# Performance work log

Measured on AMD Instinct MI355X. Metric: run time of the kernel, lower is better.

The kernel has to match this reference:

```python
import jax, jax.numpy as jnp
import numpy as np

H = 32; L = 4; HEADS = 8; VC = 16; BIG = 1e9

def _unit(v):
    return v * jax.lax.rsqrt(jnp.sum(v * v, -1, keepdims=True) + 1e-8)

def _dihedrals(bb):
    n = bb.shape[0]
    X = bb[:, :3].reshape(n * 3, 3)
    U = _unit(X[1:] - X[:-1])
    u2, u1, u0 = U[:-2], U[1:-1], U[2:]
    n2 = _unit(jnp.cross(u2, u1)); n1 = _unit(jnp.cross(u1, u0))
    cosD = jnp.clip(jnp.sum(n2 * n1, -1), -1 + 1e-6, 1 - 1e-6)
    D = jnp.sign(jnp.sum(u2 * n1, -1)) * jnp.arccos(cosD)
    D = jnp.pad(D, (1, 2)).reshape(n, 3)
    return jnp.concatenate([jnp.cos(D), jnp.sin(D)], -1)

def _orientations(x):
    f = jnp.pad(_unit(x[1:] - x[:-1]), ((0, 1), (0, 0)))
    b = jnp.pad(_unit(x[:-1] - x[1:]), ((1, 0), (0, 0)))
    return jnp.stack([f, b], -2)

def _virtual_cb(bb):
    n_, ca, c = bb[:, 0], bb[:, 1], bb[:, 2]
    b = ca - n_; cc = c - ca; a = jnp.cross(b, cc)
    return -0.58273431 * a + 0.56802827 * b - 0.54067466 * cc + ca

def _rbf(d, nbin=16, dmax=20.0):
    mu = jnp.linspace(0.0, dmax, nbin); sig = dmax / nbin
    return jnp.exp(-(((d[..., None] - mu) / sig) ** 2))

def _pos_emb(didx, nemb=16):
    freq = jnp.exp(jnp.arange(0, nemb, 2, dtype=jnp.float32) * (-np.log(10000.0) / nemb))
    ang = didx[..., None].astype(jnp.float32) * freq
    return jnp.concatenate([jnp.cos(ang), jnp.sin(ang)], -1)

def _edge_rot(vec):
    # per-edge rotation aligning edge direction to e_y (equiformer-style)
    nrm = _unit(vec)
    helper = jnp.where(jnp.abs(nrm[..., 2:3]) > 0.99, jnp.array([1.0, 0.0, 0.0]), jnp.array([0.0, 0.0, 1.0]))
    z = _unit(jnp.cross(nrm, helper))
    x = jnp.cross(nrm, z)
    return jnp.stack([x, nrm, z], axis=-2)

def _rot(R, x):
    return jnp.concatenate([x[..., :1, :], jnp.einsum('...ij,...jc->...ic', R, x[..., 1:, :])], -2)

def _rot_inv(R, x):
    return jnp.concatenate([x[..., :1, :], jnp.einsum('...ji,...jc->...ic', R, x[..., 1:, :])], -2)

def _norm_so3(x, g0, b0, g1):
    x0 = x[..., 0, :]; x1 = x[..., 1:, :]
    mu = jnp.mean(x0, -1, keepdims=True)
    var = jnp.var(x0, -1, keepdims=True)
    y0 = (x0 - mu) * jax.lax.rsqrt(var + 1e-6) * g0 + b0
    y1 = x1 * jax.lax.rsqrt(jnp.mean(x1 * x1, (-2, -1), keepdims=True) + 1e-6) * g1
    return jnp.concatenate([y0[..., None, :], y1], -2)

def _project(xin, nbr, R, ef, rw1, rw2, ow):
    src = _rot(R, xin[nbr])                         # [N,k,4,Cin] gather + rotate into edge frame
    rad = jax.nn.silu(ef @ rw1) @ rw2               # [N,k,Cin] radial weights
    msg = _rot_inv(R, src * rad[..., None, :])      # rotate back to global frame
    return jnp.mean(msg, axis=1) @ ow               # [N,4,Cout]

def _forward(bb, latent, ln_g0, ln_b0, ln_g1, bb_rad_w1, bb_rad_w2, bb_out_w,
             lat_rad_w1, lat_rad_w2, lat_out_w, tln_g0, tln_b0, tln_g1,
             attn_w1, attn_w2, v_w, o_w, ffn_w1, ffn_w2, ffn_wg, ffn_v1,
             eu_w1, eu_w2, out_rad_w1, out_rad_w2, out_w,
             seq_w1, seq_b1, seq_w2, seq_b2, seq_w3, seq_b3, x_mask, n_per, k):
    N = bb.shape[0]
    Xca = bb[:, 1]
    # backbone SO3 features [N,4,7]: l=0 dihedrals (padded to 7), l=1 seven vectors
    dih = jnp.pad(_dihedrals(bb), ((0, 0), (0, 1)))
    vecs = jnp.concatenate([bb - Xca[:, None], _orientations(Xca),
                            (_virtual_cb(bb) - Xca)[:, None]], -2)
    bb_feat = jnp.concatenate([dih[:, None, :], jnp.nan_to_num(jnp.swapaxes(vecs, -1, -2))], 1)
    # kNN graph within each chain; masked residues pushed far away
    batch = jnp.arange(N) // n_per
    mx = jnp.where(x_mask[:, None], BIG, Xca)
    sq = jnp.sum(mx * mx, -1)
    d2 = sq[:, None] + sq[None, :] - 2.0 * (mx @ mx.T)
    bad = (batch[:, None] != batch[None, :]) | jnp.eye(N, dtype=bool)
    d2 = jnp.where(bad, BIG, d2)
    _, nbr = jax.lax.top_k(-d2, k)                  # [N,k] source indices per target
    edge_vec = Xca[:, None] - Xca[nbr]
    R = _edge_rot(edge_vec)                         # [N,k,3,3]
    dist = jnp.sqrt(jnp.sum(edge_vec * edge_vec, -1) + 1e-12)
    ef = jnp.concatenate([_rbf(dist), _pos_emb(nbr - jnp.arange(N)[:, None])], -1)  # [N,k,32]
    lat = _norm_so3(latent, ln_g0, ln_b0, ln_g1)
    x = jnp.concatenate([_project(bb_feat, nbr, R, ef, bb_rad_w1, bb_rad_w2, bb_out_w),
                         _project(lat, nbr, R, ef, lat_rad_w1, lat_rad_w2, lat_out_w)], -1)  # [N,4,H]
    for l in range(L):
        xl = _norm_so3(x, tln_g0[l], tln_b0[l], tln_g1[l])
        src = xl[nbr]                               # [N,k,4,H]
        feat = jnp.concatenate([src[..., 0, :],
                                jnp.broadcast_to(xl[:, None, 0, :], src[..., 0, :].shape),
                                ef], -1)            # [N,k,3H]
        alpha = jax.nn.softmax(jax.nn.silu(feat @ attn_w1[l]) @ attn_w2[l], axis=1)  # [N,k,heads]
        v = _rot_inv(R, _rot(R, src) @ v_w[l])      # [N,k,4,heads*vc]
        v = v.reshape(N, k, 4, HEADS, VC)
        agg = jnp.einsum('nkh,nkchv->nchv', alpha, v).reshape(N, 4, HEADS * VC)
        x = x + agg @ o_w[l]
        h = jax.nn.silu(x[:, 0, :] @ ffn_w1[l])
        gate = jax.nn.sigmoid(h @ ffn_wg[l])
        x = x + jnp.concatenate([(h @ ffn_w2[l])[:, None, :],
                                 (x[:, 1:, :] @ ffn_v1[l]) * gate[:, None, :]], 1)
        e_in = jnp.concatenate([ef, x[nbr][..., 0, :],
                                jnp.broadcast_to(x[:, None, 0, :], (N, k, H))], -1)
        ef = ef + jax.nn.silu(e_in @ eu_w1[l]) @ eu_w2[l]
    atoms = _project(x, nbr, R, ef, out_rad_w1, out_rad_w2, out_w)  # [N,4,91]
    decoded_latent = jnp.swapaxes(atoms[:, 1:4, :], -1, -2)         # [N,91,3]
    hh = jax.nn.relu(x[:, 0, :] @ seq_w1 + seq_b1)
    hh = jax.nn.relu(hh @ seq_w2 + seq_b2)
    seq_logits = jax.nn.log_softmax(hh @ seq_w3 + seq_b3, -1)
    return decoded_latent, seq_logits

def setup_inputs() -> dict:
    key = jax.random.key(0)
    N = 8192; n_per = 2048; k = 30
    keys = iter(jax.random.split(key, 64))
    def W(shape):
        fan = shape[-2] if len(shape) > 1 else shape[-1]
        return (jax.random.normal(next(keys), shape) / np.sqrt(fan)).astype(jnp.float32)
    inp = {
        'bb': (jax.random.normal(next(keys), (N, 4, 3)) * 3.0).astype(jnp.float32),
        'latent': jax.random.normal(next(keys), (N, 4, H), dtype=jnp.float32),
        'ln_g0': jnp.ones((H,), jnp.float32), 'ln_b0': jnp.zeros((H,), jnp.float32), 'ln_g1': jnp.ones((H,), jnp.float32),
        'bb_rad_w1': W((H, 64)), 'bb_rad_w2': W((64, 7)), 'bb_out_w': W((7, 16)),
        'lat_rad_w1': W((H, 64)), 'lat_rad_w2': W((64, H)), 'lat_out_w': W((H, 16)),
        'tln_g0': jnp.ones((L, H), jnp.float32), 'tln_b0': jnp.zeros((L, H), jnp.float32), 'tln_g1': jnp.ones((L, H), jnp.float32),
        'attn_w1': W((L, 3 * H, H)), 'attn_w2': W((L, H, HEADS)),
        'v_w': W((L, H, HEADS * VC)), 'o_w': W((L, HEADS * VC, H)),
        'ffn_w1': W((L, H, 2 * H)), 'ffn_w2': W((L, 2 * H, H)), 'ffn_wg': W((L, 2 * H, H)), 'ffn_v1': W((L, H, H)),
        'eu_w1': W((L, 3 * H, 2 * H)), 'eu_w2': W((L, 2 * H, H)),
        'out_rad_w1': W((H, 64)), 'out_rad_w2': W((64, H)), 'out_w': W((H, 91)),
        'seq_w1': W((H, 64)), 'seq_b1': jnp.zeros((64,), jnp.float32),
        'seq_w2': W((64, H)), 'seq_b2': jnp.zeros((H,), jnp.float32),
        'seq_w3': W((H, 20)), 'seq_b3': jnp.zeros((20,), jnp.float32),
        'x_mask': jnp.zeros((N,), bool), 'n_per': n_per, 'k': k,
    }
    return inp

def reference(bb, latent, ln_g0, ln_b0, ln_g1, bb_rad_w1, bb_rad_w2, bb_out_w,
              lat_rad_w1, lat_rad_w2, lat_out_w, tln_g0, tln_b0, tln_g1,
              attn_w1, attn_w2, v_w, o_w, ffn_w1, ffn_w2, ffn_wg, ffn_v1,
              eu_w1, eu_w2, out_rad_w1, out_rad_w2, out_w,
              seq_w1, seq_b1, seq_w2, seq_b2, seq_w3, seq_b3, x_mask, n_per, k):
    return _forward(bb, latent, ln_g0, ln_b0, ln_g1, bb_rad_w1, bb_rad_w2, bb_out_w,
                    lat_rad_w1, lat_rad_w2, lat_out_w, tln_g0, tln_b0, tln_g1,
                    attn_w1, attn_w2, v_w, o_w, ffn_w1, ffn_w2, ffn_wg, ffn_v1,
                    eu_w1, eu_w2, out_rad_w1, out_rad_w2, out_w,
                    seq_w1, seq_b1, seq_w2, seq_b2, seq_w3, seq_b3, x_mask, n_per, k)
```

## Files before the change

### kernel.cpp

```cpp
#include <hip/hip_runtime.h>
#include <math.h>

#define NRES 8192
#define NPER 2048
#define KNB  30
#define NEDGE (NRES*KNB)

typedef float v2f __attribute__((ext_vector_type(2)));

__device__ __forceinline__ float siluf(float x){ return x / (1.0f + __expf(-x)); }
__device__ __forceinline__ v2f splat2(float a){ v2f r; r.x=a; r.y=a; return r; }

__global__ void k_bbfeat(const float* __restrict__ bb, float* __restrict__ bbf,
                         float4* __restrict__ ca){
  int n = blockIdx.x*256 + threadIdx.x;
  if(n >= NRES) return;
  const float* r = bb + n*12;
  float cax=r[3], cay=r[4], caz=r[5];
  ca[n] = make_float4(cax,cay,caz, cax*cax+cay*cay+caz*caz);
  float vx[7],vy[7],vz[7];
  for(int a=0;a<4;a++){ vx[a]=r[a*3]-cax; vy[a]=r[a*3+1]-cay; vz[a]=r[a*3+2]-caz; }
  if(n<NRES-1){
    float dx=bb[(n+1)*12+3]-cax, dy=bb[(n+1)*12+4]-cay, dz=bb[(n+1)*12+5]-caz;
    float s=rsqrtf(dx*dx+dy*dy+dz*dz+1e-8f);
    vx[4]=dx*s; vy[4]=dy*s; vz[4]=dz*s;
  } else { vx[4]=0.f; vy[4]=0.f; vz[4]=0.f; }
  if(n>0){
    float dx=bb[(n-1)*12+3]-cax, dy=bb[(n-1)*12+4]-cay, dz=bb[(n-1)*12+5]-caz;
    float s=rsqrtf(dx*dx+dy*dy+dz*dz+1e-8f);
    vx[5]=dx*s; vy[5]=dy*s; vz[5]=dz*s;
  } else { vx[5]=0.f; vy[5]=0.f; vz[5]=0.f; }
  {
    float bx=cax-r[0], by=cay-r[1], bz=caz-r[2];
    float cx=r[6]-cax, cy=r[7]-cay, cz=r[8]-caz;
    float axx=by*cz-bz*cy, ayy=bz*cx-bx*cz, azz=bx*cy-by*cx;
    vx[6]=-0.58273431f*axx+0.56802827f*bx-0.54067466f*cx;
    vy[6]=-0.58273431f*ayy+0.56802827f*by-0.54067466f*cy;
    vz[6]=-0.58273431f*azz+0.56802827f*bz-0.54067466f*cz;
  }
  float cD[3], sD[3];
  for(int t=0;t<3;t++){
    cD[t]=1.0f; sD[t]=0.0f;
    int f=3*n+t-1;
    if(f>=0 && f<3*NRES-3){
      float X[4][3];
      for(int q=0;q<4;q++){
        int m=f+q, rr=m/3, aa=m-rr*3;
        X[q][0]=bb[rr*12+aa*3]; X[q][1]=bb[rr*12+aa*3+1]; X[q][2]=bb[rr*12+aa*3+2];
      }
      float u2x=X[1][0]-X[0][0], u2y=X[1][1]-X[0][1], u2z=X[1][2]-X[0][2];
      float u1x=X[2][0]-X[1][0], u1y=X[2][1]-X[1][1], u1z=X[2][2]-X[1][2];
      float u0x=X[3][0]-X[2][0], u0y=X[3][1]-X[2][1], u0z=X[3][2]-X[2][2];
      float s2=rsqrtf(u2x*u2x+u2y*u2y+u2z*u2z+1e-8f); u2x*=s2; u2y*=s2; u2z*=s2;
      float s1=rsqrtf(u1x*u1x+u1y*u1y+u1z*u1z+1e-8f); u1x*=s1; u1y*=s1; u1z*=s1;
      float s0=rsqrtf(u0x*u0x+u0y*u0y+u0z*u0z+1e-8f); u0x*=s0; u0y*=s0; u0z*=s0;
      float n2x=u2y*u1z-u2z*u1y, n2y=u2z*u1x-u2x*u1z, n2z=u2x*u1y-u2y*u1x;
      float nn2=rsqrtf(n2x*n2x+n2y*n2y+n2z*n2z+1e-8f); n2x*=nn2; n2y*=nn2; n2z*=nn2;
      float n1x=u1y*u0z-u1z*u0y, n1y=u1z*u0x-u1x*u0z, n1z=u1x*u0y-u1y*u0x;
      float nn1=rsqrtf(n1x*n1x+n1y*n1y+n1z*n1z+1e-8f); n1x*=nn1; n1y*=nn1; n1z*=nn1;
      float dotn = n2x*n1x+n2y*n1y+n2z*n1z;
      float cosD = fminf(fmaxf(dotn, -1.0f+1e-6f), 1.0f-1e-6f);
      float sg = u2x*n1x+u2y*n1y+u2z*n1z;
      if(sg==0.0f){ cD[t]=1.0f; sD[t]=0.0f; }
      else {
        float sgn = (sg>0.0f)?1.0f:-1.0f;
        cD[t]=cosD;
        sD[t]=sgn*sqrtf(fmaxf(1.0f-cosD*cosD,0.0f));
      }
    }
  }
  float* o = bbf + n*28;
  o[0]=cD[0]; o[1]=cD[1]; o[2]=cD[2]; o[3]=sD[0]; o[4]=sD[1]; o[5]=sD[2]; o[6]=0.f;
  for(int c=0;c<7;c++){ o[7+c]=vx[c]; o[14+c]=vy[c]; o[21+c]=vz[c]; }
}

__device__ __forceinline__ unsigned long long knn_extract(const float* __restrict__ vals,
                                                          unsigned &mask, int lane){
  float bm=INFINITY; int ba=0;
  #pragma unroll
  for(int t=0;t<32;t++){
    if(!((mask>>t)&1u) && vals[t]<bm){ bm=vals[t]; ba=t; }
  }
  mask |= 1u<<ba;
  unsigned ub = __float_as_uint(bm);
  ub ^= (ub & 0x80000000u) ? 0xFFFFFFFFu : 0x80000000u;
  return ((unsigned long long)ub<<32) | (unsigned)(ba*64+lane);
}

__global__ __launch_bounds__(256) void k_knn(const float4* __restrict__ ca, int* __restrict__ nbr){
  __shared__ float sx[NPER], sy[NPER], sz[NPER], sq[NPER];
  int wave = threadIdx.x>>6;
  int lane = threadIdx.x&63;
  int i = blockIdx.x*4 + wave;
  int batch = i / NPER;
  int base = batch*NPER;
  for(int t=threadIdx.x; t<NPER; t+=256){
    float4 c = ca[base+t];
    sx[t]=c.x; sy[t]=c.y; sz[t]=c.z; sq[t]=c.w;
  }
  __syncthreads();
  int il = i - base;
  float xi=sx[il], yi=sy[il], zi=sz[il], si=sq[il];
  float vals[32];
  #pragma unroll
  for(int t=0;t<32;t++){
    int j = t*64 + lane;
    float d2 = si + sq[j] - 2.0f*(xi*sx[j]+yi*sy[j]+zi*sz[j]);
    if(j==il) d2 = 1e30f;
    vals[t]=d2;
  }
  unsigned mask = 0;
  unsigned long long s0 = knn_extract(vals, mask, lane);
  unsigned long long s1 = knn_extract(vals, mask, lane);
  unsigned long long s2 = knn_extract(vals, mask, lane);
  unsigned long long s3 = knn_extract(vals, mask, lane);
  const unsigned long long EMPTY = ~0ull;
  for(int it=0; it<KNB; it++){
    unsigned long long m = s0;
    #pragma unroll
    for(int off=32; off>0; off>>=1){
      unsigned long long o = __shfl_xor(m, off, 64);
      m = (o<m) ? o : m;
    }
    if(lane==0) nbr[i*KNB+it] = base + (int)(m & 0x7FFull);
    if((int)(m & 63ull) == lane){
      s0=s1; s1=s2; s2=s3; s3=EMPTY;
      if(s0==EMPTY) s0 = knn_extract(vals, mask, lane);
    }
  }
}

__global__ void k_tbl(float* __restrict__ tbl){
  int i = blockIdx.x*256 + threadIdx.x;
  int d = i>>3, m = i&7;
  float freq = __expf(-1.1512925465f*(float)m);
  float ang = (float)(d-2048)*freq;
  tbl[d*16+m]   = cosf(ang);
  tbl[d*16+8+m] = sinf(ang);
}

__global__ __launch_bounds__(128, 4)
void k_edgerad(const float4* __restrict__ ca, const int* __restrict__ nbr,
               const float* __restrict__ tbl,
               const float* __restrict__ bbw1, const float* __restrict__ bbw2,
               const float* __restrict__ latw1, const float* __restrict__ latw2,
               float* __restrict__ ef, float* __restrict__ radbb, float* __restrict__ radlat){
  int e = blockIdx.x*128 + threadIdx.x;
  int n = e/KNB;
  int j = nbr[e];
  float4 cn = ca[n], cj = ca[j];
  float dx=cn.x-cj.x, dy=cn.y-cj.y, dz=cn.z-cj.z;
  float dist = sqrtf(dx*dx+dy*dy+dz*dz + 1e-12f);
  float f[32];
  #pragma unroll
  for(int m=0;m<16;m++){
    float mu = (20.0f/15.0f)*(float)m;
    float t = (dist-mu)*(1.0f/1.25f);
    f[m] = __expf(-t*t);
  }
  {
    const float4* t4 = (const float4*)(tbl + (size_t)(j - n + 2048)*16);
    float4 c0=t4[0], c1=t4[1], s0=t4[2], s1=t4[3];
    f[16]=c0.x; f[17]=c0.y; f[18]=c0.z; f[19]=c0.w;
    f[20]=c1.x; f[21]=c1.y; f[22]=c1.z; f[23]=c1.w;
    f[24]=s0.x; f[25]=s0.y; f[26]=s0.z; f[27]=s0.w;
    f[28]=s1.x; f[29]=s1.y; f[30]=s1.z; f[31]=s1.w;
  }
  {
    float4* o4 = (float4*)(ef + (size_t)e*32);
    #pragma unroll
    for(int q=0;q<8;q++) o4[q] = make_float4(f[q*4],f[q*4+1],f[q*4+2],f[q*4+3]);
  }
  float ab[7];
  #pragma unroll
  for(int t=0;t<7;t++) ab[t]=0.f;
  #pragma unroll
  for(int half=0; half<2; half++){
    v2f h[16];
    #pragma unroll
    for(int o=0;o<16;o++) h[o]=splat2(0.f);
    #pragma unroll
    for(int c=0;c<32;c++){
      v2f fc = splat2(f[c]);
      const v2f* w = (const v2f*)(bbw1 + c*64 + half*32);
      #pragma unroll
      for(int o=0;o<16;o++) h[o] += fc*w[o];
    }
    #pragma unroll
    for(int o=0;o<16;o++){
      float v0 = siluf(h[o].x), v1 = siluf(h[o].y);
      const float* wa = bbw2 + (half*32+o*2)*7;
      const float* wb = bbw2 + (half*32+o*2+1)*7;
      #pragma unroll
      for(int t=0;t<7;t++) ab[t] += v0*wa[t];
      #pragma unroll
      for(int t=0;t<7;t++) ab[t] += v1*wb[t];
    }
  }
  {
    float4* rb4 = (float4*)(radbb + (size_t)e*8);
    rb4[0] = make_float4(ab[0],ab[1],ab[2],ab[3]);
    rb4[1] = make_float4(ab[4],ab[5],ab[6],0.f);
  }
  v2f al[16];
  #pragma unroll
  for(int t=0;t<16;t++) al[t]=splat2(0.f);
  #pragma unroll
  for(int half=0; half<2; half++){
    v2f h[16];
    #pragma unroll
    for(int o=0;o<16;o++) h[o]=splat2(0.f);
    #pragma unroll
    for(int c=0;c<32;c++){
      v2f fc = splat2(f[c]);
      const v2f* w = (const v2f*)(latw1 + c*64 + half*32);
      #pragma unroll
      for(int o=0;o<16;o++) h[o] += fc*w[o];
    }
    #pragma unroll
    for(int o=0;o<16;o++){
      float v0 = siluf(h[o].x), v1 = siluf(h[o].y);
      const v2f* wa = (const v2f*)(latw2 + (half*32+o*2)*32);
      const v2f* wb = (const v2f*)(latw2 + (half*32+o*2+1)*32);
      v2f va = splat2(v0), vb = splat2(v1);
      #pragma unroll
      for(int t=0;t<16;t++) al[t] += va*wa[t];
      #pragma unroll
      for(int t=0;t<16;t++) al[t] += vb*wb[t];
    }
  }
  v2f* rl2 = (v2f*)(radlat + (size_t)e*32);
  #pragma unroll
  for(int q=0;q<16;q++) rl2[q] = al[q];
}

__global__ void k_norm(const float* __restrict__ in, float* __restrict__ out,
                       const float* __restrict__ g0, const float* __restrict__ b0,
                       const float* __restrict__ g1){
  int tid = blockIdx.x*256 + threadIdx.x;
  int n = tid >> 5, lane = tid & 31;
  if(n >= NRES) return;
  const float* xn = in + n*128;
  float x0 = xn[lane];
  float s = x0, s2 = x0*x0;
  for(int off=16; off>0; off>>=1){ s += __shfl_xor(s, off, 32); s2 += __shfl_xor(s2, off, 32); }
  float mu = s*(1.0f/32.0f);
  float var = s2*(1.0f/32.0f) - mu*mu;
  float y0 = (x0-mu)*rsqrtf(var+1e-6f)*g0[lane] + b0[lane];
  float v1 = xn[32+lane], v2 = xn[64+lane], v3 = xn[96+lane];
  float ss = v1*v1+v2*v2+v3*v3;
  for(int off=16; off>0; off>>=1){ ss += __shfl_xor(ss, off, 32); }
  float sc = rsqrtf(ss*(1.0f/96.0f) + 1e-6f);
  float g = g1[lane];
  out[n*128+lane]     = y0;
  out[n*128+32+lane]  = v1*sc*g;
  out[n*128+64+lane]  = v2*sc*g;
  out[n*128+96+lane]  = v3*sc*g;
}

__device__ __forceinline__ void load32(float* __restrict__ f, const float* __restrict__ src){
  const float4* s4 = (const float4*)src;
  #pragma unroll
  for(int q=0;q<8;q++){
    float4 v = s4[q];
    f[q*4+0]=v.x; f[q*4+1]=v.y; f[q*4+2]=v.z; f[q*4+3]=v.w;
  }
}

__global__ __launch_bounds__(256) void k_init(const int* __restrict__ nbr,
                       const float* __restrict__ radbb, const float* __restrict__ radlat,
                       const float* __restrict__ bbf, const float* __restrict__ latn,
                       const float* __restrict__ bboutw, const float* __restrict__ latoutw,
                       const float* __restrict__ g0, const float* __restrict__ b0,
                       const float* __restrict__ g1,
                       float* __restrict__ x, float* __restrict__ xl){
  __shared__ float msgbb[4][32], msglat[4][128], xout[4][128];
  int g = threadIdx.x>>6, t = threadIdx.x&63;
  int n = blockIdx.x*4 + g;
  int t31 = t&31, t7 = t%7;
  float accL0=0.f, accL1=0.f, accB=0.f;
  for(int kk=0; kk<KNB; kk++){
    int e = n*KNB+kk;
    int j = nbr[e];
    float rl = radlat[(size_t)e*32 + t31];
    accL0 += latn[j*128+t]    * rl;
    accL1 += latn[j*128+64+t] * rl;
    if(t<28) accB += bbf[j*28+t]*radbb[(size_t)e*8 + t7];
  }
  msglat[g][t]=accL0*(1.0f/KNB); msglat[g][64+t]=accL1*(1.0f/KNB);
  if(t<28) msgbb[g][t]=accB*(1.0f/KNB);
  for(int half=0; half<2; half++){
    int e = half*64+t;
    int rrow = e>>5, c = e&31;
    float v=0.f;
    if(c<16){ for(int q=0;q<7;q++)  v += msgbb[g][rrow*7+q]*bboutw[q*16+c]; }
    else    { for(int q=0;q<32;q++) v += msglat[g][rrow*32+q]*latoutw[q*16+(c-16)]; }
    xout[g][e]=v;
    x[n*128+e]=v;
  }
  if(t<32){
    float x0=xout[g][t];
    float s=x0, s2=x0*x0;
    for(int off=16; off>0; off>>=1){ s+=__shfl_xor(s,off,32); s2+=__shfl_xor(s2,off,32); }
    float mu=s*(1.0f/32.0f), var=s2*(1.0f/32.0f)-mu*mu;
    float y0=(x0-mu)*rsqrtf(var+1e-6f)*g0[t]+b0[t];
    float v1=xout[g][32+t], v2=xout[g][64+t], v3=xout[g][96+t];
    float ss=v1*v1+v2*v2+v3*v3;
    for(int off=16; off>0; off>>=1) ss+=__shfl_xor(ss,off,32);
    float sc=rsqrtf(ss*(1.0f/96.0f)+1e-6f);
    float gg=g1[t];
    xl[n*128+t]=y0; xl[n*128+32+t]=v1*sc*gg; xl[n*128+64+t]=v2*sc*gg; xl[n*128+96+t]=v3*sc*gg;
  }
}

__global__ __launch_bounds__(256) void k_nodeprep0(const float* __restrict__ xl,
                       const float* __restrict__ aw1,
                       float* __restrict__ asrc, float* __restrict__ adst){
  __shared__ float sl[4][32];
  int g = threadIdx.x>>6, lane = threadIdx.x&63;
  int n = blockIdx.x*4 + g;
  if(lane<32) sl[g][lane] = xl[n*128+lane];
  __syncthreads();
  int o = lane&31;
  int roff = (lane>=32)? 32 : 0;
  float a=0.f;
  #pragma unroll
  for(int c=0;c<32;c++) a += sl[g][c]*aw1[(roff+c)*32+o];
  if(lane<32) asrc[n*32+o]=a; else adst[n*32+o]=a;
}

__global__ __launch_bounds__(128, 4)
void k_logits(const int* __restrict__ nbr,
              const float* __restrict__ asrc, const float* __restrict__ adst,
              const float* __restrict__ ef, const float* __restrict__ w1,
              const float* __restrict__ w2, float* __restrict__ logits){
  int e = blockIdx.x*128 + threadIdx.x;
  int n = e/KNB;
  int j = nbr[e];
  v2f h[16];
  {
    const v2f* pj = (const v2f*)(asrc + (size_t)j*32);
    const v2f* pn = (const v2f*)(adst + (size_t)n*32);
    #pragma unroll
    for(int q=0;q<16;q++) h[q] = pj[q]+pn[q];
  }
  float f[32];
  load32(f, ef + (size_t)e*32);
  #pragma unroll
  for(int c=0;c<32;c++){
    v2f fc = splat2(f[c]);
    const v2f* w = (const v2f*)(w1 + (64+c)*32);
    #pragma unroll
    for(int o=0;o<16;o++) h[o] += fc*w[o];
  }
  v2f acc[4];
  #pragma unroll
  for(int t=0;t<4;t++) acc[t]=splat2(0.f);
  #pragma unroll
  for(int o=0;o<16;o++){
    float v0 = siluf(h[o].x), v1 = siluf(h[o].y);
    const v2f* wa = (const v2f*)(w2 + (o*2)*8);
    const v2f* wb = (const v2f*)(w2 + (o*2+1)*8);
    v2f va = splat2(v0), vb = splat2(v1);
    #pragma unroll
    for(int t=0;t<4;t++) acc[t] += va*wa[t];
    #pragma unroll
    for(int t=0;t<4;t++) acc[t] += vb*wb[t];
  }
  v2f* lg2 = (v2f*)(logits + (size_t)e*8);
  #pragma unroll
  for(int q=0;q<4;q++) lg2[q] = acc[q];
}

__global__ __launch_bounds__(256) void k_update(const int* __restrict__ nbr, const float* __restrict__ xl,
                         const float* __restrict__ logits, float* __restrict__ x,
                         float* __restrict__ xlout,
                         const float* __restrict__ vw, const float* __restrict__ ow,
                         const float* __restrict__ fw1, const float* __restrict__ fw2,
                         const float* __restrict__ fwg, const float* __restrict__ fv1,
                         const float* __restrict__ g0, const float* __restrict__ b0,
                         const float* __restrict__ g1,
                         const float* __restrict__ ew1l, const float* __restrict__ aw1n,
                         float* __restrict__ hsrc, float* __restrict__ hdst,
                         float* __restrict__ asrc, float* __restrict__ adst){
  __shared__ float S_lg[4][240], S_m[4][8], S_inv[4][8];
  __shared__ float S_S[4][1024], S_agg[4][512], S_x[4][128];
  __shared__ float S_h[4][64], S_g[4][32], S_d0[4][32], S_y0[4][32];
  int g = threadIdx.x>>6, t = threadIdx.x&63;
  int n = blockIdx.x*4 + g;
  for(int r=t; r<240; r+=64) S_lg[g][r] = logits[(size_t)n*240+r];
  if(t<8){
    float m=-1e30f;
    for(int kk=0;kk<KNB;kk++) m=fmaxf(m, S_lg[g][kk*8+t]);
    float s=0.f;
    for(int kk=0;kk<KNB;kk++) s += __expf(S_lg[g][kk*8+t]-m);
    S_m[g][t]=m; S_inv[g][t]=1.0f/s;
  }
  for(int r=t; r<240; r+=64){ int h=r&7; S_lg[g][r]=__expf(S_lg[g][r]-S_m[g][h])*S_inv[g][h]; }
  int hd = t>>3, i8 = t&7;
  const float4* xl4 = (const float4*)xl;
  float acc[16];
  for(int m=0;m<16;m++) acc[m]=0.f;
  for(int kk=0;kk<KNB;kk++){
    int j=nbr[n*KNB+kk];
    float a = S_lg[g][kk*8+hd];
    float4 b0v = xl4[j*32 + i8*4 + 0];
    float4 b1v = xl4[j*32 + i8*4 + 1];
    float4 b2v = xl4[j*32 + i8*4 + 2];
    float4 b3v = xl4[j*32 + i8*4 + 3];
    acc[0]+=a*b0v.x; acc[1]+=a*b0v.y; acc[2]+=a*b0v.z; acc[3]+=a*b0v.w;
    acc[4]+=a*b1v.x; acc[5]+=a*b1v.y; acc[6]+=a*b1v.z; acc[7]+=a*b1v.w;
    acc[8]+=a*b2v.x; acc[9]+=a*b2v.y; acc[10]+=a*b2v.z; acc[11]+=a*b2v.w;
    acc[12]+=a*b3v.x; acc[13]+=a*b3v.y; acc[14]+=a*b3v.z; acc[15]+=a*b3v.w;
  }
  for(int m=0;m<16;m++) S_S[g][hd*128 + i8*16 + m] = acc[m];
  for(int half=0; half<2; half++){
    int hv = half*64+t;
    int hh = hv>>4;
    float a0=0.f,a1=0.f,a2=0.f,a3=0.f;
    for(int c=0;c<32;c++){
      float w = vw[c*128+hv];
      a0 += S_S[g][hh*128 + c]*w;
      a1 += S_S[g][hh*128 + 32+c]*w;
      a2 += S_S[g][hh*128 + 64+c]*w;
      a3 += S_S[g][hh*128 + 96+c]*w;
    }
    S_agg[g][hv]=a0; S_agg[g][128+hv]=a1; S_agg[g][256+hv]=a2; S_agg[g][384+hv]=a3;
  }
  for(int half=0; half<2; half++){
    int e = half*64+t;
    int rrow = e>>5, c = e&31;
    float v = x[n*128+e];
    for(int hv=0;hv<128;hv++) v += S_agg[g][rrow*128+hv]*ow[hv*32+c];
    S_x[g][e]=v;
  }
  {
    float hs=0.f;
    for(int c=0;c<32;c++) hs += S_x[g][c]*fw1[c*64+t];
    S_h[g][t]=siluf(hs);
  }
  if(t<32){
    float gs=0.f, d0=0.f;
    for(int c=0;c<64;c++){ float hv=S_h[g][c]; gs += hv*fwg[c*32+t]; d0 += hv*fw2[c*32+t]; }
    S_g[g][t]=1.0f/(1.0f+__expf(-gs));
    S_d0[g][t]=d0;
  }
  for(int half=0; half<2; half++){
    int e = half*64+t;
    int rrow = e>>5, c = e&31;
    float xv = S_x[g][e], outv;
    if(rrow==0){ outv = xv + S_d0[g][c]; }
    else {
      float dv=0.f;
      for(int cc=0;cc<32;cc++) dv += S_x[g][rrow*32+cc]*fv1[cc*32+c];
      outv = xv + dv*S_g[g][c];
    }
    S_x[g][e]=outv;
    x[n*128+e]=outv;
  }
  if(t<32){
    float x0=S_x[g][t];
    float s=x0, s2=x0*x0;
    for(int off=16; off>0; off>>=1){ s+=__shfl_xor(s,off,32); s2+=__shfl_xor(s2,off,32); }
    float mu=s*(1.0f/32.0f), var=s2*(1.0f/32.0f)-mu*mu;
    float y0=(x0-mu)*rsqrtf(var+1e-6f)*g0[t]+b0[t];
    float v1=S_x[g][32+t], v2=S_x[g][64+t], v3=S_x[g][96+t];
    float ss=v1*v1+v2*v2+v3*v3;
    for(int off=16; off>0; off>>=1) ss+=__shfl_xor(ss,off,32);
    float sc=rsqrtf(ss*(1.0f/96.0f)+1e-6f);
    float gg=g1[t];
    xlout[n*128+t]=y0; xlout[n*128+32+t]=v1*sc*gg;
    xlout[n*128+64+t]=v2*sc*gg; xlout[n*128+96+t]=v3*sc*gg;
    S_y0[g][t]=y0;
  }
  {
    float a0=0.f, a1=0.f;
    #pragma unroll
    for(int c=0;c<32;c++){
      float xv = S_x[g][c];
      a0 += xv*ew1l[(32+c)*64+t];
      a1 += xv*ew1l[(64+c)*64+t];
    }
    hsrc[n*64+t]=a0; hdst[n*64+t]=a1;
  }
  if(aw1n){
    int o = t&31;
    int roff = (t>=32)? 32 : 0;
    float a=0.f;
    #pragma unroll
    for(int c=0;c<32;c++) a += S_y0[g][c]*aw1n[(roff+c)*32+o];
    if(t<32) asrc[n*32+o]=a; else adst[n*32+o]=a;
  }
}

__global__ __launch_bounds__(128, 4)
void k_efup(const int* __restrict__ nbr,
            const float* __restrict__ hsrc, const float* __restrict__ hdst,
            const float* __restrict__ ew1, const float* __restrict__ ew2,
            float* __restrict__ ef,
            const float* __restrict__ asrc, const float* __restrict__ adst,
            const float* __restrict__ aw1n, const float* __restrict__ aw2n,
            float* __restrict__ logits){
  int e = blockIdx.x*128 + threadIdx.x;
  int n = e/KNB;
  int j = nbr[e];
  float f[32];
  load32(f, ef + (size_t)e*32);
  v2f acc[16];
  #pragma unroll
  for(int t=0;t<16;t++) acc[t]=splat2(0.f);
  #pragma unroll
  for(int half=0; half<2; half++){
    v2f h[16];
    {
      const v2f* pj = (const v2f*)(hsrc + (size_t)j*64 + half*32);
      const v2f* pn = (const v2f*)(hdst + (size_t)n*64 + half*32);
      #pragma unroll
      for(int q=0;q<16;q++) h[q] = pj[q]+pn[q];
    }
    #pragma unroll
    for(int c=0;c<32;c++){
      v2f fc = splat2(f[c]);
      const v2f* w = (const v2f*)(ew1 + c*64 + half*32);
      #pragma unroll
      for(int o=0;o<16;o++) h[o] += fc*w[o];
    }
    #pragma unroll
    for(int o=0;o<16;o++){
      float v0 = siluf(h[o].x), v1 = siluf(h[o].y);
      const v2f* wa = (const v2f*)(ew2 + (half*32+o*2)*32);
      const v2f* wb = (const v2f*)(ew2 + (half*32+o*2+1)*32);
      v2f va = splat2(v0), vb = splat2(v1);
      #pragma unroll
      for(int t=0;t<16;t++) acc[t] += va*wa[t];
      #pragma unroll
      for(int t=0;t<16;t++) acc[t] += vb*wb[t];
    }
  }
  #pragma unroll
  for(int t=0;t<16;t++){ f[2*t] += acc[t].x; f[2*t+1] += acc[t].y; }
  float4* e4 = (float4*)(ef + (size_t)e*32);
  #pragma unroll
  for(int q=0;q<8;q++)
    e4[q] = make_float4(f[q*4+0], f[q*4+1], f[q*4+2], f[q*4+3]);
  v2f h2[16];
  {
    const v2f* pj = (const v2f*)(asrc + (size_t)j*32);
    const v2f* pn = (const v2f*)(adst + (size_t)n*32);
    #pragma unroll
    for(int q=0;q<16;q++) h2[q] = pj[q]+pn[q];
  }
  #pragma unroll
  for(int c=0;c<32;c++){
    v2f fc = splat2(f[c]);
    const v2f* w = (const v2f*)(aw1n + (64+c)*32);
    #pragma unroll
    for(int o=0;o<16;o++) h2[o] += fc*w[o];
  }
  v2f a8[4];
  #pragma unroll
  for(int t=0;t<4;t++) a8[t]=splat2(0.f);
  #pragma unroll
  for(int o=0;o<16;o++){
    float v0 = siluf(h2[o].x), v1 = siluf(h2[o].y);
    const v2f* wa = (const v2f*)(aw2n + (o*2)*8);
    const v2f* wb = (const v2f*)(aw2n + (o*2+1)*8);
    v2f va = splat2(v0), vb = splat2(v1);
    #pragma unroll
    for(int t=0;t<4;t++) a8[t] += va*wa[t];
    #pragma unroll
    for(int t=0;t<4;t++) a8[t] += vb*wb[t];
  }
  v2f* lg2 = (v2f*)(logits + (size_t)e*8);
  #pragma unroll
  for(int q=0;q<4;q++) lg2[q] = a8[q];
}

__global__ __launch_bounds__(128, 4)
void k_efup_orad(const int* __restrict__ nbr,
                 const float* __restrict__ hsrc, const float* __restrict__ hdst,
                 const float* __restrict__ ew1, const float* __restrict__ ew2,
                 float* __restrict__ ef,
                 const float* __restrict__ orw1, const float* __restrict__ orw2){
  int e = blockIdx.x*128 + threadIdx.x;
  int n = e/KNB;
  int j = nbr[e];
  float f[32];
  load32(f, ef + (size_t)e*32);
  v2f acc[16];
  #pragma unroll
  for(int t=0;t<16;t++) acc[t]=splat2(0.f);
  #pragma unroll
  for(int half=0; half<2; half++){
    v2f h[16];
    {
      const v2f* pj = (const v2f*)(hsrc + (size_t)j*64 + half*32);
      const v2f* pn = (const v2f*)(hdst + (size_t)n*64 + half*32);
      #pragma unroll
      for(int q=0;q<16;q++) h[q] = pj[q]+pn[q];
    }
    #pragma unroll
    for(int c=0;c<32;c++){
      v2f fc = splat2(f[c]);
      const v2f* w = (const v2f*)(ew1 + c*64 + half*32);
      #pragma unroll
      for(int o=0;o<16;o++) h[o] += fc*w[o];
    }
    #pragma unroll
    for(int o=0;o<16;o++){
      float v0 = siluf(h[o].x), v1 = siluf(h[o].y);
      const v2f* wa = (const v2f*)(ew2 + (half*32+o*2)*32);
      const v2f* wb = (const v2f*)(ew2 + (half*32+o*2+1)*32);
      v2f va = splat2(v0), vb = splat2(v1);
      #pragma unroll
      for(int t=0;t<16;t++) acc[t] += va*wa[t];
      #pragma unroll
      for(int t=0;t<16;t++) acc[t] += vb*wb[t];
    }
  }
  #pragma unroll
  for(int t=0;t<16;t++){ f[2*t] += acc[t].x; f[2*t+1] += acc[t].y; }
  v2f oa[16];
  #pragma unroll
  for(int t=0;t<16;t++) oa[t]=splat2(0.f);
  #pragma unroll
  for(int half=0; half<2; half++){
    v2f h[16];
    #pragma unroll
    for(int o=0;o<16;o++) h[o]=splat2(0.f);
    #pragma unroll
    for(int c=0;c<32;c++){
      v2f fc = splat2(f[c]);
      const v2f* w = (const v2f*)(orw1 + c*64 + half*32);
      #pragma unroll
      for(int o=0;o<16;o++) h[o] += fc*w[o];
    }
    #pragma unroll
    for(int o=0;o<16;o++){
      float v0 = siluf(h[o].x), v1 = siluf(h[o].y);
      const v2f* wa = (const v2f*)(orw2 + (half*32+o*2)*32);
      const v2f* wb = (const v2f*)(orw2 + (half*32+o*2+1)*32);
      v2f va = splat2(v0), vb = splat2(v1);
      #pragma unroll
      for(int t=0;t<16;t++) oa[t] += va*wa[t];
      #pragma unroll
      for(int t=0;t<16;t++) oa[t] += vb*wb[t];
    }
  }
  v2f* r2 = (v2f*)(ef + (size_t)e*32);
  #pragma unroll
  for(int q=0;q<16;q++) r2[q] = oa[q];
}

__global__ __launch_bounds__(256) void k_out(const int* __restrict__ nbr, const float* __restrict__ orad,
                      const float* __restrict__ x,
                      const float* __restrict__ outw,
                      const float* __restrict__ sw1, const float* __restrict__ sb1,
                      const float* __restrict__ sw2, const float* __restrict__ sb2,
                      const float* __restrict__ sw3, const float* __restrict__ sb3,
                      float* __restrict__ out, float* __restrict__ outseq){
  __shared__ float msg[4][128];
  __shared__ float h1[4][64], h2[4][32], lgs[4][20];
  int g = threadIdx.x>>6, t = threadIdx.x&63;
  int n = blockIdx.x*4 + g;
  int t31 = t&31;
  float acc0=0.f, acc1=0.f;
  for(int kk=0;kk<KNB;kk++){
    int e=n*KNB+kk;
    int j=nbr[e];
    float rl = orad[(size_t)e*32 + t31];
    acc0 += x[j*128+t]*rl;
    acc1 += x[j*128+64+t]*rl;
  }
  msg[g][t]=acc0*(1.0f/KNB); msg[g][64+t]=acc1*(1.0f/KNB);
  for(int o=t;o<91;o+=64){
    for(int rrow=1;rrow<4;rrow++){
      float s=0.f;
      for(int c=0;c<32;c++) s += msg[g][rrow*32+c]*outw[c*91+o];
      out[(size_t)n*273 + o*3 + (rrow-1)] = s;
    }
  }
  {
    float s=0.f;
    for(int c=0;c<32;c++) s += x[n*128+c]*sw1[c*64+t];
    h1[g][t]=fmaxf(s+sb1[t],0.f);
  }
  if(t<32){
    float s=0.f;
    for(int c=0;c<64;c++) s += h1[g][c]*sw2[c*32+t];
    h2[g][t]=fmaxf(s+sb2[t],0.f);
  }
  if(t<20){
    float s=0.f;
    for(int c=0;c<32;c++) s += h2[g][c]*sw3[c*20+t];
    lgs[g][t]=s+sb3[t];
  }
  if(t<20){
    float m=-1e30f;
    for(int c=0;c<20;c++) m=fmaxf(m,lgs[g][c]);
    float se=0.f;
    for(int c=0;c<20;c++) se += __expf(lgs[g][c]-m);
    outseq[(size_t)n*20+t]=lgs[g][t]-m-logf(se);
  }
}

extern "C" void kernel_launch(void* const* d_in, const int* in_sizes, int n_in,
                              void* d_out, int out_size, void* d_ws, size_t ws_size,
                              hipStream_t stream) {
  const float* bb      = (const float*)d_in[0];
  const float* latent  = (const float*)d_in[1];
  const float* ln_g0   = (const float*)d_in[2];
  const float* ln_b0   = (const float*)d_in[3];
  const float* ln_g1   = (const float*)d_in[4];
  const float* bbw1    = (const float*)d_in[5];
  const float* bbw2    = (const float*)d_in[6];
  const float* bboutw  = (const float*)d_in[7];
  const float* latw1   = (const float*)d_in[8];
  const float* latw2   = (const float*)d_in[9];
  const float* latoutw = (const float*)d_in[10];
  const float* tg0     = (const float*)d_in[11];
  const float* tb0     = (const float*)d_in[12];
  const float* tg1     = (const float*)d_in[13];
  const float* aw1     = (const float*)d_in[14];
  const float* aw2     = (const float*)d_in[15];
  const float* vw      = (const float*)d_in[16];
  const float* ow      = (const float*)d_in[17];
  const float* fw1     = (const float*)d_in[18];
  const float* fw2     = (const float*)d_in[19];
  const float* fwg     = (const float*)d_in[20];
  const float* fv1     = (const float*)d_in[21];
  const float* ew1     = (const float*)d_in[22];
  const float* ew2     = (const float*)d_in[23];
  const float* orw1    = (const float*)d_in[24];
  const float* orw2    = (const float*)d_in[25];
  const float* outw    = (const float*)d_in[26];
  const float* sw1     = (const float*)d_in[27];
  const float* sb1     = (const float*)d_in[28];
  const float* sw2     = (const float*)d_in[29];
  const float* sb2     = (const float*)d_in[30];
  const float* sw3     = (const float*)d_in[31];
  const float* sb3     = (const float*)d_in[32];
  float* outp = (float*)d_out;

  int*    nbr    = (int*)d_ws;
  float*  ef     = (float*)((char*)d_ws + 1024*1024);
  float*  xbuf   = ef   + (size_t)NEDGE*32;
  float*  xlA    = xbuf + (size_t)NRES*128;
  float*  xlB    = xlA  + (size_t)NRES*128;
  float*  bbf    = xlB  + (size_t)NRES*128;
  float*  logits = bbf  + (size_t)NRES*28;
  float4* ca     = (float4*)(logits + (size_t)NEDGE*8);
  float*  edgescratch = (float*)(ca + NRES);
  float*  radbb  = logits;
  float*  radlat = edgescratch;
  float*  tbl    = xbuf;
  float*  hsrc   = edgescratch;
  float*  hdst   = edgescratch + (size_t)NRES*64;
  float*  asrc   = edgescratch + (size_t)NRES*128;
  float*  adst   = edgescratch + (size_t)NRES*128 + (size_t)NRES*32;

  k_bbfeat  <<<NRES/256, 256, 0, stream>>>(bb, bbf, ca);
  k_knn     <<<NRES/4,   256, 0, stream>>>(ca, nbr);
  k_tbl     <<<4096*8/256, 256, 0, stream>>>(tbl);
  k_edgerad <<<NEDGE/128, 128, 0, stream>>>(ca, nbr, tbl, bbw1, bbw2, latw1, latw2,
                                            ef, radbb, radlat);
  k_norm    <<<NRES*32/256, 256, 0, stream>>>(latent, xlA, ln_g0, ln_b0, ln_g1);
  k_init    <<<NRES/4, 256, 0, stream>>>(nbr, radbb, radlat, bbf, xlA,
                                         bboutw, latoutw,
                                         tg0, tb0, tg1,
                                         xbuf, xlB);
  k_nodeprep0<<<NRES/4, 256, 0, stream>>>(xlB, aw1, asrc, adst);
  k_logits   <<<NEDGE/128, 128, 0, stream>>>(nbr, asrc, adst, ef, aw1, aw2, logits);
  for(int l=0;l<4;l++){
    const float* xl_in  = (l&1) ? xlA : xlB;
    float*       xl_out = (l&1) ? xlB : xlA;
    int ln = (l+1<4) ? (l+1) : 3;
    const float* aw1n = (l<3) ? (aw1+(l+1)*96*32) : nullptr;
    k_update <<<NRES/4, 256, 0, stream>>>(nbr, xl_in, logits, xbuf, xl_out,
                                          vw+l*32*128, ow+l*128*32,
                                          fw1+l*32*64, fw2+l*64*32,
                                          fwg+l*64*32, fv1+l*32*32,
                                          tg0+ln*32, tb0+ln*32, tg1+ln*32,
                                          ew1+l*96*64, aw1n,
                                          hsrc, hdst, asrc, adst);
    if(l<3){
      k_efup<<<NEDGE/128, 128, 0, stream>>>(nbr, hsrc, hdst,
                                            ew1+l*96*64, ew2+l*64*32, ef,
                                            asrc, adst,
                                            aw1+(l+1)*96*32, aw2+(l+1)*32*8, logits);
    } else {
      k_efup_orad<<<NEDGE/128, 128, 0, stream>>>(nbr, hsrc, hdst,
                                                 ew1+l*96*64, ew2+l*64*32, ef,
                                                 orw1, orw2);
    }
  }
  k_out <<<NRES/4, 256, 0, stream>>>(nbr, ef , xbuf, outw,
                                     sw1, sb1, sw2, sb2, sw3, sb3,
                                     outp, outp + (size_t)NRES*273);
}
```

Before: 1.210 ms.

## Split edge feature and radial kernels, move node projections out of update kernel

Splits k_edgerad into a light edge-feature kernel and a separate radial-MLP kernel that reloads features from memory. It also moves the per-node hsrc/hdst/asrc/adst projections out of k_update into a standalone k_nodeprep kernel launched after each update. k_efup now stages the edge features in shared memory and processes the hidden layer in four quarters instead of two halves. The aim is lower register pressure and higher occupancy in the heavy kernels, at the cost of extra kernel launches and extra global memory round trips.

```diff
diff --git a/kernel.cpp b/kernel.cpp
--- a/kernel.cpp
+++ b/kernel.cpp
@@ -139,13 +139,10 @@
   tbl[d*16+8+m] = sinf(ang);
 }
 
-__global__ __launch_bounds__(128, 4)
-void k_edgerad(const float4* __restrict__ ca, const int* __restrict__ nbr,
-               const float* __restrict__ tbl,
-               const float* __restrict__ bbw1, const float* __restrict__ bbw2,
-               const float* __restrict__ latw1, const float* __restrict__ latw2,
-               float* __restrict__ ef, float* __restrict__ radbb, float* __restrict__ radlat){
-  int e = blockIdx.x*128 + threadIdx.x;
+__global__ void k_edgefeat(const float4* __restrict__ ca, const int* __restrict__ nbr,
+                           const float* __restrict__ tbl, float* __restrict__ ef){
+  int e = blockIdx.x*256 + threadIdx.x;
+  if(e >= NEDGE) return;
   int n = e/KNB;
   int j = nbr[e];
   float4 cn = ca[n], cj = ca[j];
@@ -166,72 +163,9 @@
     f[24]=s0.x; f[25]=s0.y; f[26]=s0.z; f[27]=s0.w;
     f[28]=s1.x; f[29]=s1.y; f[30]=s1.z; f[31]=s1.w;
   }
-  {
-    float4* o4 = (float4*)(ef + (size_t)e*32);
-    #pragma unroll
-    for(int q=0;q<8;q++) o4[q] = make_float4(f[q*4],f[q*4+1],f[q*4+2],f[q*4+3]);
-  }
-  float ab[7];
-  #pragma unroll
-  for(int t=0;t<7;t++) ab[t]=0.f;
-  #pragma unroll
-  for(int half=0; half<2; half++){
-    v2f h[16];
-    #pragma unroll
-    for(int o=0;o<16;o++) h[o]=splat2(0.f);
-    #pragma unroll
-    for(int c=0;c<32;c++){
-      v2f fc = splat2(f[c]);
-      const v2f* w = (const v2f*)(bbw1 + c*64 + half*32);
-      #pragma unroll
-      for(int o=0;o<16;o++) h[o] += fc*w[o];
-    }
-    #pragma unroll
-    for(int o=0;o<16;o++){
-      float v0 = siluf(h[o].x), v1 = siluf(h[o].y);
-      const float* wa = bbw2 + (half*32+o*2)*7;
-      const float* wb = bbw2 + (half*32+o*2+1)*7;
-      #pragma unroll
-      for(int t=0;t<7;t++) ab[t] += v0*wa[t];
-      #pragma unroll
-      for(int t=0;t<7;t++) ab[t] += v1*wb[t];
-    }
-  }
-  {
-    float4* rb4 = (float4*)(radbb + (size_t)e*8);
-    rb4[0] = make_float4(ab[0],ab[1],ab[2],ab[3]);
-    rb4[1] = make_float4(ab[4],ab[5],ab[6],0.f);
-  }
-  v2f al[16];
-  #pragma unroll
-  for(int t=0;t<16;t++) al[t]=splat2(0.f);
-  #pragma unroll
-  for(int half=0; half<2; half++){
-    v2f h[16];
-    #pragma unroll
-    for(int o=0;o<16;o++) h[o]=splat2(0.f);
-    #pragma unroll
-    for(int c=0;c<32;c++){
-      v2f fc = splat2(f[c]);
-      const v2f* w = (const v2f*)(latw1 + c*64 + half*32);
-      #pragma unroll
-      for(int o=0;o<16;o++) h[o] += fc*w[o];
-    }
-    #pragma unroll
-    for(int o=0;o<16;o++){
-      float v0 = siluf(h[o].x), v1 = siluf(h[o].y);
-      const v2f* wa = (const v2f*)(latw2 + (half*32+o*2)*32);
-      const v2f* wb = (const v2f*)(latw2 + (half*32+o*2+1)*32);
-      v2f va = splat2(v0), vb = splat2(v1);
-      #pragma unroll
-      for(int t=0;t<16;t++) al[t] += va*wa[t];
-      #pragma unroll
-      for(int t=0;t<16;t++) al[t] += vb*wb[t];
-    }
-  }
-  v2f* rl2 = (v2f*)(radlat + (size_t)e*32);
-  #pragma unroll
-  for(int q=0;q<16;q++) rl2[q] = al[q];
+  float4* o4 = (float4*)(ef + (size_t)e*32);
+  #pragma unroll
+  for(int q=0;q<8;q++) o4[q] = make_float4(f[q*4],f[q*4+1],f[q*4+2],f[q*4+3]);
 }
 
 __global__ void k_norm(const float* __restrict__ in, float* __restrict__ out,
@@ -267,6 +201,77 @@
   }
 }
 
+__global__ __launch_bounds__(128, 4)
+void k_rad(const float* __restrict__ ef,
+           const float* __restrict__ bbw1, const float* __restrict__ bbw2,
+           const float* __restrict__ latw1, const float* __restrict__ latw2,
+           float* __restrict__ radbb, float* __restrict__ radlat){
+  int e = blockIdx.x*128 + threadIdx.x;
+  float f[32];
+  load32(f, ef + (size_t)e*32);
+  float ab[7];
+  #pragma unroll
+  for(int t=0;t<7;t++) ab[t]=0.f;
+  #pragma unroll
+  for(int half=0; half<2; half++){
+    v2f h[16];
+    #pragma unroll
+    for(int o=0;o<16;o++) h[o]=splat2(0.f);
+    #pragma unroll
+    for(int c=0;c<32;c++){
+      v2f fc = splat2(f[c]);
+      const v2f* w = (const v2f*)(bbw1 + c*64 + half*32);
+      #pragma unroll
+      for(int o=0;o<16;o++) h[o] += fc*w[o];
+    }
+    #pragma unroll
+    for(int o=0;o<16;o++){
+      float v0 = siluf(h[o].x), v1 = siluf(h[o].y);
+      const float* wa = bbw2 + (half*32+o*2)*7;
+      const float* wb = bbw2 + (half*32+o*2+1)*7;
+      #pragma unroll
+      for(int t=0;t<7;t++) ab[t] += v0*wa[t];
+      #pragma unroll
+      for(int t=0;t<7;t++) ab[t] += v1*wb[t];
+    }
+  }
+  {
+    float4* rb4 = (float4*)(radbb + (size_t)e*8);
+    rb4[0] = make_float4(ab[0],ab[1],ab[2],ab[3]);
+    rb4[1] = make_float4(ab[4],ab[5],ab[6],0.f);
+  }
+  v2f al[16];
+  #pragma unroll
+  for(int t=0;t<16;t++) al[t]=splat2(0.f);
+  #pragma unroll
+  for(int half=0; half<2; half++){
+    v2f h[16];
+    #pragma unroll
+    for(int o=0;o<16;o++) h[o]=splat2(0.f);
+    #pragma unroll
+    for(int c=0;c<32;c++){
+      v2f fc = splat2(f[c]);
+      const v2f* w = (const v2f*)(latw1 + c*64 + half*32);
+      #pragma unroll
+      for(int o=0;o<16;o++) h[o] += fc*w[o];
+    }
+    #pragma unroll
+    for(int o=0;o<16;o++){
+      float v0 = siluf(h[o].x), v1 = siluf(h[o].y);
+      const v2f* wa = (const v2f*)(latw2 + (half*32+o*2)*32);
+      const v2f* wb = (const v2f*)(latw2 + (half*32+o*2+1)*32);
+      v2f va = splat2(v0), vb = splat2(v1);
+      #pragma unroll
+      for(int t=0;t<16;t++) al[t] += va*wa[t];
+      #pragma unroll
+      for(int t=0;t<16;t++) al[t] += vb*wb[t];
+    }
+  }
+  v2f* rl2 = (v2f*)(radlat + (size_t)e*32);
+  #pragma unroll
+  for(int q=0;q<16;q++) rl2[q] = al[q];
+}
+
 __global__ __launch_bounds__(256) void k_init(const int* __restrict__ nbr,
                        const float* __restrict__ radbb, const float* __restrict__ radlat,
                        const float* __restrict__ bbf, const float* __restrict__ latn,
@@ -313,20 +318,37 @@
   }
 }
 
-__global__ __launch_bounds__(256) void k_nodeprep0(const float* __restrict__ xl,
-                       const float* __restrict__ aw1,
+__global__ __launch_bounds__(256) void k_nodeprep(const float* __restrict__ x,
+                       const float* __restrict__ xl,
+                       const float* __restrict__ ew1, const float* __restrict__ aw1,
+                       float* __restrict__ hsrc, float* __restrict__ hdst,
                        float* __restrict__ asrc, float* __restrict__ adst){
-  __shared__ float sl[4][32];
+  __shared__ float sx[4][32], sl[4][32];
   int g = threadIdx.x>>6, lane = threadIdx.x&63;
   int n = blockIdx.x*4 + g;
-  if(lane<32) sl[g][lane] = xl[n*128+lane];
+  if(lane<32){
+    if(x)   sx[g][lane] = x[n*128+lane];
+    if(aw1) sl[g][lane] = xl[n*128+lane];
+  }
   __syncthreads();
-  int o = lane&31;
-  int roff = (lane>=32)? 32 : 0;
-  float a=0.f;
-  #pragma unroll
-  for(int c=0;c<32;c++) a += sl[g][c]*aw1[(roff+c)*32+o];
-  if(lane<32) asrc[n*32+o]=a; else adst[n*32+o]=a;
+  if(x){
+    float a0=0.f, a1=0.f;
+    #pragma unroll
+    for(int c=0;c<32;c++){
+      float xv = sx[g][c];
+      a0 += xv*ew1[(32+c)*64+lane];
+      a1 += xv*ew1[(64+c)*64+lane];
+    }
+    hsrc[n*64+lane]=a0; hdst[n*64+lane]=a1;
+  }
+  if(aw1){
+    int o = lane&31;
+    int roff = (lane>=32)? 32 : 0;
+    float a=0.f;
+    #pragma unroll
+    for(int c=0;c<32;c++) a += sl[g][c]*aw1[(roff+c)*32+o];
+    if(lane<32) asrc[n*32+o]=a; else adst[n*32+o]=a;
+  }
 }
 
 __global__ __launch_bounds__(128, 4)
@@ -379,13 +401,10 @@
                          const float* __restrict__ fw1, const float* __restrict__ fw2,
                          const float* __restrict__ fwg, const float* __restrict__ fv1,
                          const float* __restrict__ g0, const float* __restrict__ b0,
-                         const float* __restrict__ g1,
-                         const float* __restrict__ ew1l, const float* __restrict__ aw1n,
-                         float* __restrict__ hsrc, float* __restrict__ hdst,
-                         float* __restrict__ asrc, float* __restrict__ adst){
+                         const float* __restrict__ g1){
   __shared__ float S_lg[4][240], S_m[4][8], S_inv[4][8];
   __shared__ float S_S[4][1024], S_agg[4][512], S_x[4][128];
-  __shared__ float S_h[4][64], S_g[4][32], S_d0[4][32], S_y0[4][32];
+  __shared__ float S_h[4][64], S_g[4][32], S_d0[4][32];
   int g = threadIdx.x>>6, t = threadIdx.x&63;
   int n = blockIdx.x*4 + g;
   for(int r=t; r<240; r+=64) S_lg[g][r] = logits[(size_t)n*240+r];
@@ -471,25 +490,6 @@
     float gg=g1[t];
     xlout[n*128+t]=y0; xlout[n*128+32+t]=v1*sc*gg;
     xlout[n*128+64+t]=v2*sc*gg; xlout[n*128+96+t]=v3*sc*gg;
-    S_y0[g][t]=y0;
-  }
-  {
-    float a0=0.f, a1=0.f;
-    #pragma unroll
-    for(int c=0;c<32;c++){
-      float xv = S_x[g][c];
-      a0 += xv*ew1l[(32+c)*64+t];
-      a1 += xv*ew1l[(64+c)*64+t];
-    }
-    hsrc[n*64+t]=a0; hdst[n*64+t]=a1;
-  }
-  if(aw1n){
-    int o = t&31;
-    int roff = (t>=32)? 32 : 0;
-    float a=0.f;
-    #pragma unroll
-    for(int c=0;c<32;c++) a += S_y0[g][c]*aw1n[(roff+c)*32+o];
-    if(t<32) asrc[n*32+o]=a; else adst[n*32+o]=a;
   }
 }
 
@@ -501,35 +501,47 @@
             const float* __restrict__ asrc, const float* __restrict__ adst,
             const float* __restrict__ aw1n, const float* __restrict__ aw2n,
             float* __restrict__ logits){
-  int e = blockIdx.x*128 + threadIdx.x;
+  __shared__ float Sf[128][33];
+  int tl = threadIdx.x;
+  int e = blockIdx.x*128 + tl;
   int n = e/KNB;
   int j = nbr[e];
-  float f[32];
-  load32(f, ef + (size_t)e*32);
+  {
+    const float4* s4 = (const float4*)(ef + (size_t)e*32);
+    #pragma unroll
+    for(int q=0;q<8;q++){
+      float4 v = s4[q];
+      Sf[tl][q*4+0]=v.x; Sf[tl][q*4+1]=v.y; Sf[tl][q*4+2]=v.z; Sf[tl][q*4+3]=v.w;
+    }
+  }
   v2f acc[16];
   #pragma unroll
   for(int t=0;t<16;t++) acc[t]=splat2(0.f);
   #pragma unroll
-  for(int half=0; half<2; half++){
-    v2f h[16];
+  for(int oq=0; oq<4; oq++){
+    v2f h[8];
     {
-      const v2f* pj = (const v2f*)(hsrc + (size_t)j*64 + half*32);
-      const v2f* pn = (const v2f*)(hdst + (size_t)n*64 + half*32);
-      #pragma unroll
-      for(int q=0;q<16;q++) h[q] = pj[q]+pn[q];
+      const float4* pj = (const float4*)(hsrc + (size_t)j*64 + oq*16);
+      const float4* pn = (const float4*)(hdst + (size_t)n*64 + oq*16);
+      #pragma unroll
+      for(int q=0;q<4;q++){
+        float4 a=pj[q], b=pn[q];
+        h[2*q]   = (v2f){a.x+b.x, a.y+b.y};
+        h[2*q+1] = (v2f){a.z+b.z, a.w+b.w};
+      }
     }
     #pragma unroll
     for(int c=0;c<32;c++){
-      v2f fc = splat2(f[c]);
-      const v2f* w = (const v2f*)(ew1 + c*64 + half*32);
-      #pragma unroll
-      for(int o=0;o<16;o++) h[o] += fc*w[o];
-    }
-    #pragma unroll
-    for(int o=0;o<16;o++){
+      v2f fc = splat2(Sf[tl][c]);
+      const v2f* w = (const v2f*)(ew1 + c*64 + oq*16);
+      #pragma unroll
+      for(int o=0;o<8;o++) h[o] += fc*w[o];
+    }
+    #pragma unroll
+    for(int o=0;o<8;o++){
       float v0 = siluf(h[o].x), v1 = siluf(h[o].y);
-      const v2f* wa = (const v2f*)(ew2 + (half*32+o*2)*32);
-      const v2f* wb = (const v2f*)(ew2 + (half*32+o*2+1)*32);
+      const v2f* wa = (const v2f*)(ew2 + (oq*16+o*2)*32);
+      const v2f* wb = (const v2f*)(ew2 + (oq*16+o*2+1)*32);
       v2f va = splat2(v0), vb = splat2(v1);
       #pragma unroll
       for(int t=0;t<16;t++) acc[t] += va*wa[t];
@@ -537,12 +549,18 @@
       for(int t=0;t<16;t++) acc[t] += vb*wb[t];
     }
   }
-  #pragma unroll
-  for(int t=0;t<16;t++){ f[2*t] += acc[t].x; f[2*t+1] += acc[t].y; }
-  float4* e4 = (float4*)(ef + (size_t)e*32);
-  #pragma unroll
-  for(int q=0;q<8;q++)
-    e4[q] = make_float4(f[q*4+0], f[q*4+1], f[q*4+2], f[q*4+3]);
+  {
+    float4* e4 = (float4*)(ef + (size_t)e*32);
+    #pragma unroll
+    for(int q=0;q<8;q++){
+      float f0 = Sf[tl][q*4+0] + acc[2*q].x;
+      float f1 = Sf[tl][q*4+1] + acc[2*q].y;
+      float f2 = Sf[tl][q*4+2] + acc[2*q+1].x;
+      float f3 = Sf[tl][q*4+3] + acc[2*q+1].y;
+      e4[q] = make_float4(f0,f1,f2,f3);
+      Sf[tl][q*4+0]=f0; Sf[tl][q*4+1]=f1; Sf[tl][q*4+2]=f2; Sf[tl][q*4+3]=f3;
+    }
+  }
   v2f h2[16];
   {
     const v2f* pj = (const v2f*)(asrc + (size_t)j*32);
@@ -552,7 +570,7 @@
   }
   #pragma unroll
   for(int c=0;c<32;c++){
-    v2f fc = splat2(f[c]);
+    v2f fc = splat2(Sf[tl][c]);
     const v2f* w = (const v2f*)(aw1n + (64+c)*32);
     #pragma unroll
     for(int o=0;o<16;o++) h2[o] += fc*w[o];
@@ -762,33 +780,34 @@
   k_bbfeat  <<<NRES/256, 256, 0, stream>>>(bb, bbf, ca);
   k_knn     <<<NRES/4,   256, 0, stream>>>(ca, nbr);
   k_tbl     <<<4096*8/256, 256, 0, stream>>>(tbl);
-  k_edgerad <<<NEDGE/128, 128, 0, stream>>>(ca, nbr, tbl, bbw1, bbw2, latw1, latw2,
-                                            ef, radbb, radlat);
+  k_edgefeat<<<NEDGE/256, 256, 0, stream>>>(ca, nbr, tbl, ef);
   k_norm    <<<NRES*32/256, 256, 0, stream>>>(latent, xlA, ln_g0, ln_b0, ln_g1);
+  k_rad     <<<NEDGE/128, 128, 0, stream>>>(ef, bbw1, bbw2, latw1, latw2, radbb, radlat);
   k_init    <<<NRES/4, 256, 0, stream>>>(nbr, radbb, radlat, bbf, xlA,
                                          bboutw, latoutw,
                                          tg0, tb0, tg1,
                                          xbuf, xlB);
-  k_nodeprep0<<<NRES/4, 256, 0, stream>>>(xlB, aw1, asrc, adst);
-  k_logits   <<<NEDGE/128, 128, 0, stream>>>(nbr, asrc, adst, ef, aw1, aw2, logits);
+  k_nodeprep<<<NRES/4, 256, 0, stream>>>(nullptr, xlB, ew1, aw1, hsrc, hdst, asrc, adst);
+  k_logits  <<<NEDGE/128, 128, 0, stream>>>(nbr, asrc, adst, ef, aw1, aw2, logits);
   for(int l=0;l<4;l++){
     const float* xl_in  = (l&1) ? xlA : xlB;
     float*       xl_out = (l&1) ? xlB : xlA;
     int ln = (l+1<4) ? (l+1) : 3;
-    const float* aw1n = (l<3) ? (aw1+(l+1)*96*32) : nullptr;
     k_update <<<NRES/4, 256, 0, stream>>>(nbr, xl_in, logits, xbuf, xl_out,
                                           vw+l*32*128, ow+l*128*32,
                                           fw1+l*32*64, fw2+l*64*32,
                                           fwg+l*64*32, fv1+l*32*32,
-                                          tg0+ln*32, tb0+ln*32, tg1+ln*32,
-                                          ew1+l*96*64, aw1n,
-                                          hsrc, hdst, asrc, adst);
+                                          tg0+ln*32, tb0+ln*32, tg1+ln*32);
     if(l<3){
+      k_nodeprep<<<NRES/4, 256, 0, stream>>>(xbuf, xl_out, ew1+l*96*64, aw1+(l+1)*96*32,
+                                             hsrc, hdst, asrc, adst);
       k_efup<<<NEDGE/128, 128, 0, stream>>>(nbr, hsrc, hdst,
                                             ew1+l*96*64, ew2+l*64*32, ef,
                                             asrc, adst,
                                             aw1+(l+1)*96*32, aw2+(l+1)*32*8, logits);
     } else {
+      k_nodeprep<<<NRES/4, 256, 0, stream>>>(xbuf, xl_out, ew1+l*96*64, nullptr,
+                                             hsrc, hdst, asrc, adst);
       k_efup_orad<<<NEDGE/128, 128, 0, stream>>>(nbr, hsrc, hdst,
                                                  ew1+l*96*64, ew2+l*64*32, ef,
                                                  orw1, orw2);
```

Measured after the change: 1.140 ms. -5.8%, faster.
